# Optimization experiments

Measured on AMD Instinct MI355X. Metric: run time of the kernel, lower is better.

Reference implementation:

```python
import jax, jax.numpy as jnp
import numpy as np

B, C, H, W = 8, 512, 64, 64
KD, VD, OD = 64, 512, 512
BN_EPS = 1e-5


def setup_inputs() -> dict:
    key = jax.random.key(0)
    ks = jax.random.split(key, 10)
    s = lambda fan_in: 1.0 / np.sqrt(fan_in)
    return {
        "x": jax.random.normal(ks[0], (B, C, H, W), jnp.float32),
        "Wq": jax.random.normal(ks[1], (KD, C), jnp.float32) * s(C),
        "bq": jnp.zeros((KD,), jnp.float32),
        "Wk": jax.random.normal(ks[2], (KD, C), jnp.float32) * s(C),
        "bk": jnp.zeros((KD,), jnp.float32),
        "Wv": jax.random.normal(ks[3], (VD, C), jnp.float32) * s(C),
        "bv": jnp.zeros((VD,), jnp.float32),
        "gamma": jnp.zeros((1,), jnp.float32),  # torch init: zeros(1)
        "Wf": jax.random.normal(ks[4], (OD, VD), jnp.float32) * s(VD),
        "bn_w": jnp.ones((OD,), jnp.float32),
        "bn_b": jnp.zeros((OD,), jnp.float32),
        "bn_mean": jnp.zeros((OD,), jnp.float32),
        "bn_var": jnp.ones((OD,), jnp.float32),
    }


def reference(x, Wq, bq, Wk, bk, Wv, bv, gamma, Wf, bn_w, bn_b, bn_mean, bn_var):
    b, c, h, w = x.shape
    n = h * w
    # 1x1 convs == per-pixel channel matmuls
    q = jnp.einsum('bchw,kc->bkhw', x, Wq) + bq[None, :, None, None]  # [B,KD,H,W]
    k = jnp.einsum('bchw,kc->bkhw', x, Wk) + bk[None, :, None, None]
    v = jnp.einsum('bchw,vc->bvhw', x, Wv) + bv[None, :, None, None]
    q = q.reshape(b, -1, n)  # [B,KD,N]
    k = k.reshape(b, -1, n)
    v = v.reshape(b, -1, n)  # [B,VD,N]
    # energy[b, i, j] = q[:, :, i] . k[:, :, j]   (proj_query permuted)
    energy = jnp.einsum('bki,bkj->bij', q, k)  # [B,N,N]
    attention = jax.nn.softmax(energy, axis=-1)
    # out = value @ attention^T : out[b, v, i] = sum_j value[b, v, j] * attention[b, i, j]
    out = jnp.einsum('bvj,bij->bvi', v, attention)  # [B,VD,N]
    out = out.reshape(b, c, h, w)
    out = gamma * out + x
    # fuse: 1x1 conv (no bias) -> BatchNorm (inference) -> ReLU
    fused = jnp.einsum('bchw,oc->bohw', out, Wf)
    inv = jax.lax.rsqrt(bn_var + BN_EPS)
    fused = (fused - bn_mean[None, :, None, None]) * (bn_w * inv)[None, :, None, None] + bn_b[None, :, None, None]
    return jax.nn.relu(fused)
```

## Files before the change

kernel.cpp:

```cpp
#include <hip/hip_runtime.h>
#include <hip/hip_bf16.h>

typedef unsigned short u16;
typedef unsigned int u32;
typedef __attribute__((ext_vector_type(8))) short bf16x8;
typedef __attribute__((ext_vector_type(4))) float f32x4;
typedef __attribute__((ext_vector_type(4))) u16 u16x4;

#define B_ 8
#define C_ 512
#define N_ 4096
#define KD_ 64
#define VD_ 512
#define OD_ 512

static __device__ __forceinline__ float bf2f(u16 u) {
    union { u32 i; float f; } z; z.i = ((u32)u) << 16; return z.f;
}
static __device__ __forceinline__ u16 f2bf(float f) {
    union { float f; u32 u; } v; v.f = f;
    u32 r = v.u + 0x7fffu + ((v.u >> 16) & 1u);
    return (u16)(r >> 16);
}
static __device__ __forceinline__ int swz(int row) { return ((row >> 2) + (row >> 4)) & 3; }

static __device__ __forceinline__ void tile_barrier() {
    asm volatile("s_waitcnt lgkmcnt(0)" ::: "memory");
    __builtin_amdgcn_s_barrier();
    asm volatile("" ::: "memory");
}

__global__ __launch_bounds__(256) void transpose_convert_kernel(
    const float* __restrict__ x, const float* __restrict__ Wf,
    u16* __restrict__ xT, u16* __restrict__ Wf16)
{
    const int t = threadIdx.x;
    if (blockIdx.x >= 1024) {
        const int tid = (blockIdx.x - 1024) * 256 + t;
        const float4* src = (const float4*)Wf + (size_t)tid * 16;
        u16* dst = Wf16 + (size_t)tid * 64;
        #pragma unroll
        for (int j = 0; j < 16; j++) {
            const float4 f = src[j];
            u16x4 p;
            p[0] = f2bf(f.x); p[1] = f2bf(f.y); p[2] = f2bf(f.z); p[3] = f2bf(f.w);
            *(u16x4*)(dst + j * 4) = p;
        }
        return;
    }
    __shared__ u32 tile[64][33];
    for (int it = 0; it < 4; it++) {
        const int bid = it * 1024 + blockIdx.x;
        const int nt = bid & 63;
        const int ct = (bid >> 6) & 7;
        const int b  = bid >> 9;
        const float* xb  = x  + ((size_t)b * C_ + ct * 64) * N_ + nt * 64;
        u16*         xTb = xT + ((size_t)b * N_ + nt * 64) * C_ + ct * 64;
        {
            const int p  = t >> 3;
            const int n8 = t & 7;
            const float* r0 = xb + (size_t)(2 * p)     * N_ + n8 * 8;
            const float* r1 = xb + (size_t)(2 * p + 1) * N_ + n8 * 8;
            const float4 a0 = *(const float4*)(r0);
            const float4 a1 = *(const float4*)(r0 + 4);
            const float4 c0 = *(const float4*)(r1);
            const float4 c1 = *(const float4*)(r1 + 4);
            const float av[8] = { a0.x, a0.y, a0.z, a0.w, a1.x, a1.y, a1.z, a1.w };
            const float cv[8] = { c0.x, c0.y, c0.z, c0.w, c1.x, c1.y, c1.z, c1.w };
            #pragma unroll
            for (int j = 0; j < 8; j++)
                tile[n8 * 8 + j][p] = (u32)f2bf(av[j]) | ((u32)f2bf(cv[j]) << 16);
        }
        __syncthreads();
        #pragma unroll
        for (int h = 0; h < 2; h++) {
            const int id = t + h * 256;
            const int n  = id >> 3;
            const int q  = id & 7;
            uint4 val;
            val.x = tile[n][q * 4 + 0];
            val.y = tile[n][q * 4 + 1];
            val.z = tile[n][q * 4 + 2];
            val.w = tile[n][q * 4 + 3];
            *(uint4*)(xTb + (size_t)n * C_ + q * 8) = val;
        }
        __syncthreads();
    }
}

__global__ __launch_bounds__(256) void proj_kernel(
    const u16* __restrict__ xT,
    const float* __restrict__ Wq, const float* __restrict__ bq,
    const float* __restrict__ Wk, const float* __restrict__ bk,
    const float* __restrict__ Wv, const float* __restrict__ bv,
    const float* __restrict__ gamma,
    u16* __restrict__ q, u16* __restrict__ k, u16* __restrict__ v)
{
    if (gamma[0] == 0.0f) return;
    for (int it = 0; it < 2; it++) {
        const int bid = it * 256 + blockIdx.x;
        const int b = bid >> 6;
        const int p = (bid & 63) * 64 + (threadIdx.x & 63);
        const int dg = threadIdx.x >> 6;
        const u16* xrow = xT + ((size_t)b * N_ + p) * C_;
        for (int d0 = dg * 160; d0 < dg * 160 + 160; d0++) {
            const float* wrow; float bias; u16* dst; int dd; int dim;
            if (d0 < 64)       { dd = d0;       wrow = Wq + (size_t)dd * C_; bias = bq[dd]; dst = q; dim = KD_; }
            else if (d0 < 128) { dd = d0 - 64;  wrow = Wk + (size_t)dd * C_; bias = bk[dd]; dst = k; dim = KD_; }
            else               { dd = d0 - 128; wrow = Wv + (size_t)dd * C_; bias = bv[dd]; dst = v; dim = VD_; }
            float s = bias;
            for (int c = 0; c < C_; c++) s += bf2f(xrow[c]) * wrow[c];
            dst[((size_t)b * dim + dd) * N_ + p] = f2bf(s);
        }
    }
}

__global__ __launch_bounds__(256) void attn_kernel(
    const u16* __restrict__ xT, const u16* __restrict__ q,
    const u16* __restrict__ k, const u16* __restrict__ v,
    const float* __restrict__ gamma, u16* __restrict__ yT)
{
    const float g = gamma[0];
    if (g == 0.0f) return;
    __shared__ float pls[4][64];
    const int wv = threadIdx.x >> 6, lane = threadIdx.x & 63;
    for (int it = 0; it < 4; it++) {
        const int bid = it * 256 + blockIdx.x;
        const int b  = bid >> 7;
        const int q0 = (bid & 127) * 32 + wv * 8;
        const u16* kb = k + (size_t)b * KD_ * N_;
        const u16* vb = v + (size_t)b * VD_ * N_;
        for (int qi = 0; qi < 8; qi++) {
            const int i = q0 + qi;
            const float qv = bf2f(q[((size_t)b * KD_ + lane) * N_ + i]);
            float mx = -1e30f, l = 0.f;
            for (int jb = 0; jb < N_; jb += 64) {
                float e = 0.f;
                for (int kd = 0; kd < 64; kd++)
                    e += __shfl(qv, kd) * bf2f(kb[(size_t)kd * N_ + jb + lane]);
                const float nm = fmaxf(mx, e);
                l = l * __expf(mx - nm) + __expf(e - nm);
                mx = nm;
            }
            for (int off = 32; off; off >>= 1) {
                const float mo = __shfl_xor(mx, off);
                const float lo = __shfl_xor(l, off);
                const float nm = fmaxf(mx, mo);
                l = l * __expf(mx - nm) + lo * __expf(mo - nm);
                mx = nm;
            }
            float oacc[8];
            #pragma unroll
            for (int r = 0; r < 8; r++) oacc[r] = 0.f;
            for (int jb = 0; jb < N_; jb += 64) {
                float e = 0.f;
                for (int kd = 0; kd < 64; kd++)
                    e += __shfl(qv, kd) * bf2f(kb[(size_t)kd * N_ + jb + lane]);
                __syncthreads();
                pls[wv][lane] = __expf(e - mx);
                __syncthreads();
                for (int jj = 0; jj < 64; jj++) {
                    const float p = pls[wv][jj];
                    #pragma unroll
                    for (int r = 0; r < 8; r++)
                        oacc[r] += p * bf2f(vb[(size_t)(r * 64 + lane) * N_ + jb + jj]);
                }
            }
            const float inv = 1.f / l;
            #pragma unroll
            for (int r = 0; r < 8; r++) {
                const size_t idx = ((size_t)b * N_ + i) * C_ + r * 64 + lane;
                yT[idx] = f2bf(g * oacc[r] * inv + bf2f(xT[idx]));
            }
        }
    }
}

__global__ __launch_bounds__(256, 2) void gemm_bn_relu(
    const u16* __restrict__ xT, const u16* __restrict__ yT,
    const u16* __restrict__ Wf16, const float* __restrict__ gamma,
    const float* __restrict__ bnw, const float* __restrict__ bnb,
    const float* __restrict__ bnm, const float* __restrict__ bnv,
    float* __restrict__ out)
{
    __shared__ u16 lds_w[8 * 128 * 32];

    const int bid = blockIdx.x;
    const int pt8 = bid & 7;
    const int ot  = (bid >> 3) & 3;
    const int g   = bid >> 5;
    const int pt  = (g & 3) * 8 + pt8;
    const int b   = g >> 2;

    const int t = threadIdx.x;
    const int lane = t & 63;
    const int wv = t >> 6;
    const int wm = wv >> 1;
    const int wn = wv & 1;
    const int lcol = lane & 15;
    const int kq = lane >> 4;

    const int rw = t >> 2, posw = t & 3;
    const int ql = (posw - swz(rw)) & 3;
    const u16* WT0 = Wf16 + (size_t)(ot * 128 + rw) * C_ + ql * 8;
    const u16* WT1 = WT0 + (size_t)64 * C_;
    const int wla0 = rw * 32 + posw * 8;
    const int wla1 = wla0 + 64 * 32;

    int baddr[4];
    #pragma unroll
    for (int i = 0; i < 4; i++) {
        const int R = wn * 64 + i * 16 + lcol;
        baddr[i] = R * 32 + ((kq + swz(R)) & 3) * 8;
    }

    const u16* Asrc = (gamma[0] == 0.0f) ? xT : yT;
    const u16* Ab[4];
    #pragma unroll
    for (int mi = 0; mi < 4; mi++)
        Ab[mi] = Asrc + ((size_t)b * N_ + pt * 128 + wm * 64 + mi * 16 + lcol) * C_ + kq * 8;

    f32x4 acc[4][4];
    #pragma unroll
    for (int i = 0; i < 4; i++)
        #pragma unroll
        for (int j = 0; j < 4; j++)
            acc[i][j] = (f32x4){0.f, 0.f, 0.f, 0.f};

    auto loadA = [&](bf16x8 (&d)[4], int ks) {
        #pragma unroll
        for (int mi = 0; mi < 4; mi++)
            d[mi] = *(const bf16x8*)(Ab[mi] + ks * 32);
    };
    auto stepf = [&](bf16x8 (&af)[4], int ks) {
        const int kt = ks & 7;
        bf16x8 bfg[4];
        #pragma unroll
        for (int ni = 0; ni < 4; ni++)
            bfg[ni] = *(const bf16x8*)&lds_w[kt * 4096 + baddr[ni]];
        #pragma unroll
        for (int mi = 0; mi < 4; mi++)
            #pragma unroll
            for (int ni = 0; ni < 4; ni++)
                acc[mi][ni] = __builtin_amdgcn_mfma_f32_16x16x32_bf16(
                    af[mi], bfg[ni], acc[mi][ni], 0, 0, 0);
    };
    auto stageW = [&](int half) {
        #pragma unroll
        for (int kt = 0; kt < 8; kt++) {
            const uint4 w0 = *(const uint4*)(WT0 + (half * 8 + kt) * 32);
            const uint4 w1 = *(const uint4*)(WT1 + (half * 8 + kt) * 32);
            *(uint4*)&lds_w[kt * 4096 + wla0] = w0;
            *(uint4*)&lds_w[kt * 4096 + wla1] = w1;
        }
    };

    bf16x8 s0[4], s1[4], s2[4], s3[4];
    loadA(s0, 0); loadA(s1, 1); loadA(s2, 2); loadA(s3, 3);
    stageW(0);
    tile_barrier();
    stepf(s0, 0);  loadA(s0, 4);
    stepf(s1, 1);  loadA(s1, 5);
    stepf(s2, 2);  loadA(s2, 6);
    stepf(s3, 3);  loadA(s3, 7);
    stepf(s0, 4);  loadA(s0, 8);
    stepf(s1, 5);  loadA(s1, 9);
    stepf(s2, 6);  loadA(s2, 10);
    stepf(s3, 7);  loadA(s3, 11);
    tile_barrier();
    stageW(1);
    tile_barrier();
    stepf(s0, 8);  loadA(s0, 12);
    stepf(s1, 9);  loadA(s1, 13);
    stepf(s2, 10); loadA(s2, 14);
    stepf(s3, 11); loadA(s3, 15);
    stepf(s0, 12);
    stepf(s1, 13);
    stepf(s2, 14);
    stepf(s3, 15);

    float scale[4], shift[4];
    #pragma unroll
    for (int ni = 0; ni < 4; ni++) {
        const int o = ot * 128 + wn * 64 + ni * 16 + lcol;
        const float s = bnw[o] * rsqrtf(bnv[o] + 1e-5f);
        scale[ni] = s;
        shift[ni] = bnb[o] - bnm[o] * s;
    }
    #pragma unroll
    for (int mi = 0; mi < 4; mi++) {
        const int npix = pt * 128 + wm * 64 + mi * 16 + kq * 4;
        #pragma unroll
        for (int ni = 0; ni < 4; ni++) {
            const int o = ot * 128 + wn * 64 + ni * 16 + lcol;
            f32x4 pk;
            #pragma unroll
            for (int r = 0; r < 4; r++)
                pk[r] = fmaxf(acc[mi][ni][r] * scale[ni] + shift[ni], 0.0f);
            *(f32x4*)(out + ((size_t)b * OD_ + o) * N_ + npix) = pk;
        }
    }
}

extern "C" void kernel_launch(void* const* d_in, const int* in_sizes, int n_in,
                              void* d_out, int out_size, void* d_ws, size_t ws_size,
                              hipStream_t stream) {
    const float* x     = (const float*)d_in[0];
    const float* Wq    = (const float*)d_in[1];
    const float* bq    = (const float*)d_in[2];
    const float* Wk    = (const float*)d_in[3];
    const float* bk    = (const float*)d_in[4];
    const float* Wv    = (const float*)d_in[5];
    const float* bv    = (const float*)d_in[6];
    const float* gamma = (const float*)d_in[7];
    const float* Wf    = (const float*)d_in[8];
    const float* bnw   = (const float*)d_in[9];
    const float* bnb   = (const float*)d_in[10];
    const float* bnm   = (const float*)d_in[11];
    const float* bnv   = (const float*)d_in[12];
    float* out = (float*)d_out;

    char* ws = (char*)d_ws;
    u16* Wf16 = (u16*)(ws);
    u16* xT   = (u16*)(ws + 524288);
    u16* yT   = (u16*)(ws + 34078720);
    u16* q    = (u16*)(ws + 67633152);
    u16* k    = (u16*)(ws + 71827456);
    u16* v    = (u16*)(ws + 76021760);

    transpose_convert_kernel<<<1040, 256, 0, stream>>>(x, Wf, xT, Wf16);
    proj_kernel<<<256, 256, 0, stream>>>(xT, Wq, bq, Wk, bk, Wv, bv, gamma, q, k, v);
    attn_kernel<<<256, 256, 0, stream>>>(xT, q, k, v, gamma, yT);
    gemm_bn_relu<<<1024, 256, 0, stream>>>(xT, yT, Wf16, gamma, bnw, bnb, bnm, bnv, out);
}
```

Measured before the change: 179.7 us.

## Stage both GEMM operands in LDS via direct global-to-LDS loads

Rewrites the final 1x1-conv+BN+ReLU GEMM so that both the activation tile and the weight tile go through LDS using global_load_lds, one 32-wide k-slice per iteration with two barriers. Before, A was loaded straight to registers with a four-deep software prefetch and W was staged in two large halves. The change shrinks LDS use, raises the occupancy hint to 3 blocks per CU and remaps block indices so weight tiles are shared across neighbouring blocks. In exchange it drops the register prefetch pipeline, so each k-step now waits for its loads and pays barrier latency, with no double buffering.

```diff
diff --git a/kernel.cpp b/kernel.cpp
--- a/kernel.cpp
+++ b/kernel.cpp
@@ -24,10 +24,11 @@
 }
 static __device__ __forceinline__ int swz(int row) { return ((row >> 2) + (row >> 4)) & 3; }
 
-static __device__ __forceinline__ void tile_barrier() {
-    asm volatile("s_waitcnt lgkmcnt(0)" ::: "memory");
-    __builtin_amdgcn_s_barrier();
-    asm volatile("" ::: "memory");
+static __device__ __forceinline__ void gld16(const u16* g, u16* l) {
+    __builtin_amdgcn_global_load_lds(
+        (const __attribute__((address_space(1))) void*)(const void*)g,
+        (__attribute__((address_space(3))) void*)(void*)l,
+        16, 0, 0);
 }
 
 __global__ __launch_bounds__(256) void transpose_convert_kernel(
@@ -176,21 +177,21 @@
     }
 }
 
-__global__ __launch_bounds__(256, 2) void gemm_bn_relu(
+__global__ __launch_bounds__(256, 3) void gemm_bn_relu(
     const u16* __restrict__ xT, const u16* __restrict__ yT,
     const u16* __restrict__ Wf16, const float* __restrict__ gamma,
     const float* __restrict__ bnw, const float* __restrict__ bnb,
     const float* __restrict__ bnm, const float* __restrict__ bnv,
     float* __restrict__ out)
 {
-    __shared__ u16 lds_w[8 * 128 * 32];
-
-    const int bid = blockIdx.x;
-    const int pt8 = bid & 7;
-    const int ot  = (bid >> 3) & 3;
-    const int g   = bid >> 5;
-    const int pt  = (g & 3) * 8 + pt8;
-    const int b   = g >> 2;
+    __shared__ u16 lds_a[128 * 32];
+    __shared__ u16 lds_b[128 * 32];
+
+    const int wg = (blockIdx.x & 7) * 128 + (blockIdx.x >> 3);
+    const int ot = wg & 3;
+    const int mt = wg >> 2;
+    const int b  = mt >> 5;
+    const int px0 = (mt & 31) * 128;
 
     const int t = threadIdx.x;
     const int lane = t & 63;
@@ -200,26 +201,27 @@
     const int lcol = lane & 15;
     const int kq = lane >> 4;
 
-    const int rw = t >> 2, posw = t & 3;
-    const int ql = (posw - swz(rw)) & 3;
-    const u16* WT0 = Wf16 + (size_t)(ot * 128 + rw) * C_ + ql * 8;
-    const u16* WT1 = WT0 + (size_t)64 * C_;
-    const int wla0 = rw * 32 + posw * 8;
-    const int wla1 = wla0 + 64 * 32;
-
-    int baddr[4];
+    const int rs = t >> 2, ps = t & 3;
+    const int ql = (ps - swz(rs)) & 3;
+    const u16* Asrc = (gamma[0] == 0.0f) ? xT : yT;
+    const u16* ga0 = Asrc + ((size_t)(b * N_ + px0 + rs)) * C_ + ql * 8;
+    const u16* ga1 = ga0 + (size_t)64 * C_;
+    const u16* gb0 = Wf16 + ((size_t)(ot * 128 + rs)) * C_ + ql * 8;
+    const u16* gb1 = gb0 + (size_t)64 * C_;
+    u16* la0 = lds_a + wv * 512;
+    u16* la1 = lds_a + 2048 + wv * 512;
+    u16* lb0 = lds_b + wv * 512;
+    u16* lb1 = lds_b + 2048 + wv * 512;
+
+    int aaddr[4], baddr[4];
     #pragma unroll
     for (int i = 0; i < 4; i++) {
+        const int P = wm * 64 + i * 16 + lcol;
+        aaddr[i] = P * 32 + ((kq + swz(P)) & 3) * 8;
         const int R = wn * 64 + i * 16 + lcol;
         baddr[i] = R * 32 + ((kq + swz(R)) & 3) * 8;
     }
 
-    const u16* Asrc = (gamma[0] == 0.0f) ? xT : yT;
-    const u16* Ab[4];
-    #pragma unroll
-    for (int mi = 0; mi < 4; mi++)
-        Ab[mi] = Asrc + ((size_t)b * N_ + pt * 128 + wm * 64 + mi * 16 + lcol) * C_ + kq * 8;
-
     f32x4 acc[4][4];
     #pragma unroll
     for (int i = 0; i < 4; i++)
@@ -227,57 +229,28 @@
         for (int j = 0; j < 4; j++)
             acc[i][j] = (f32x4){0.f, 0.f, 0.f, 0.f};
 
-    auto loadA = [&](bf16x8 (&d)[4], int ks) {
+    #pragma unroll
+    for (int ks = 0; ks < 16; ++ks) {
+        gld16(ga0 + ks * 32, la0);
+        gld16(ga1 + ks * 32, la1);
+        gld16(gb0 + ks * 32, lb0);
+        gld16(gb1 + ks * 32, lb1);
+        __syncthreads();
+        bf16x8 af[4], bfg[4];
         #pragma unroll
         for (int mi = 0; mi < 4; mi++)
-            d[mi] = *(const bf16x8*)(Ab[mi] + ks * 32);
-    };
-    auto stepf = [&](bf16x8 (&af)[4], int ks) {
-        const int kt = ks & 7;
-        bf16x8 bfg[4];
+            af[mi] = *(const bf16x8*)&lds_a[aaddr[mi]];
         #pragma unroll
         for (int ni = 0; ni < 4; ni++)
-            bfg[ni] = *(const bf16x8*)&lds_w[kt * 4096 + baddr[ni]];
+            bfg[ni] = *(const bf16x8*)&lds_b[baddr[ni]];
         #pragma unroll
         for (int mi = 0; mi < 4; mi++)
             #pragma unroll
             for (int ni = 0; ni < 4; ni++)
                 acc[mi][ni] = __builtin_amdgcn_mfma_f32_16x16x32_bf16(
                     af[mi], bfg[ni], acc[mi][ni], 0, 0, 0);
-    };
-    auto stageW = [&](int half) {
-        #pragma unroll
-        for (int kt = 0; kt < 8; kt++) {
-            const uint4 w0 = *(const uint4*)(WT0 + (half * 8 + kt) * 32);
-            const uint4 w1 = *(const uint4*)(WT1 + (half * 8 + kt) * 32);
-            *(uint4*)&lds_w[kt * 4096 + wla0] = w0;
-            *(uint4*)&lds_w[kt * 4096 + wla1] = w1;
-        }
-    };
-
-    bf16x8 s0[4], s1[4], s2[4], s3[4];
-    loadA(s0, 0); loadA(s1, 1); loadA(s2, 2); loadA(s3, 3);
-    stageW(0);
-    tile_barrier();
-    stepf(s0, 0);  loadA(s0, 4);
-    stepf(s1, 1);  loadA(s1, 5);
-    stepf(s2, 2);  loadA(s2, 6);
-    stepf(s3, 3);  loadA(s3, 7);
-    stepf(s0, 4);  loadA(s0, 8);
-    stepf(s1, 5);  loadA(s1, 9);
-    stepf(s2, 6);  loadA(s2, 10);
-    stepf(s3, 7);  loadA(s3, 11);
-    tile_barrier();
-    stageW(1);
-    tile_barrier();
-    stepf(s0, 8);  loadA(s0, 12);
-    stepf(s1, 9);  loadA(s1, 13);
-    stepf(s2, 10); loadA(s2, 14);
-    stepf(s3, 11); loadA(s3, 15);
-    stepf(s0, 12);
-    stepf(s1, 13);
-    stepf(s2, 14);
-    stepf(s3, 15);
+        __syncthreads();
+    }
 
     float scale[4], shift[4];
     #pragma unroll
@@ -289,7 +262,7 @@
     }
     #pragma unroll
     for (int mi = 0; mi < 4; mi++) {
-        const int npix = pt * 128 + wm * 64 + mi * 16 + kq * 4;
+        const int npix = px0 + wm * 64 + mi * 16 + kq * 4;
         #pragma unroll
         for (int ni = 0; ni < 4; ni++) {
             const int o = ot * 128 + wn * 64 + ni * 16 + lcol;
```

Result: faster. 164.8 us (-8.3%).
